# Kernel tuning notes

Hardware: AMD Instinct MI355X
Metric: run time of the kernel (lower is better)

The kernel has to match this reference:

```python
import jax, jax.numpy as jnp
from jax import lax
import numpy as np

B, S, D, P = 32, 1024, 512, 20  # batch, seq_len, feature_dim, positioning_embedding


def setup_inputs() -> dict:
    key = jax.random.key(0)
    ks = jax.random.split(key, 10)
    s = 0.1  # param scale
    return {
        "x": jax.random.normal(ks[0], (B, S, D), jnp.float32),
        "pad_lengths": jnp.full((B,), S, dtype=jnp.int32),
        # LSTM params (torch gate order i,f,g,o)
        "W_ih": jax.random.normal(ks[1], (4 * P, D), jnp.float32) * s,
        "W_hh": jax.random.normal(ks[2], (4 * P, P), jnp.float32) * s,
        "b_ih": jax.random.normal(ks[3], (4 * P,), jnp.float32) * s,
        "b_hh": jax.random.normal(ks[4], (4 * P,), jnp.float32) * s,
        # mu_generator: Linear(P, 3); sigma_generator: Linear(P, 1)
        "W_mu": jax.random.normal(ks[5], (3, P), jnp.float32) * s,
        "b_mu": jax.random.normal(ks[6], (3,), jnp.float32) * s,
        "W_sigma": jax.random.normal(ks[7], (1, P), jnp.float32) * s,
        "b_sigma": jax.random.normal(ks[8], (1,), jnp.float32) * s,
    }


def _lstm(x, W_ih, W_hh, b_ih, b_hh):
    # x: [B, S, D] -> hidden states [B, S, P] (torch nn.LSTM, batch_first)
    b, _, _ = x.shape
    h0 = jnp.zeros((b, P), x.dtype)
    c0 = jnp.zeros((b, P), x.dtype)

    def step(carry, xt):
        h, c = carry
        gates = xt @ W_ih.T + h @ W_hh.T + b_ih + b_hh  # [B, 4P]
        i, f, g, o = jnp.split(gates, 4, axis=-1)
        i = jax.nn.sigmoid(i)
        f = jax.nn.sigmoid(f)
        g = jnp.tanh(g)
        o = jax.nn.sigmoid(o)
        c = f * c + i * g
        h = o * jnp.tanh(c)
        return (h, c), h

    _, hs = lax.scan(step, (h0, c0), jnp.swapaxes(x, 0, 1))  # hs: [S, B, P]
    return jnp.swapaxes(hs, 0, 1)


def reference(x, pad_lengths, W_ih, W_hh, b_ih, b_hh, W_mu, b_mu, W_sigma, b_sigma):
    b, s, _ = x.shape
    invL = 1.0 / pad_lengths.astype(jnp.float32)  # [B]

    pw = _lstm(x, W_ih, W_hh, b_ih, b_hh)                    # [B, S, P]
    mu_w = jax.nn.relu(pw @ W_mu.T + b_mu)                    # [B, S, 3]
    sigma = jax.nn.sigmoid(pw @ W_sigma.T + b_sigma)[..., 0]  # [B, S]

    # Sequential mu recurrence: mu_j = max(mw0*prev_mu + mw1/L + mw2*(j+1)/L, j/L)
    js = jnp.arange(s, dtype=jnp.float32)

    def mu_step(prev_mu, inp):
        mw, j = inp  # mw: [B, 3]
        mu = mw[:, 0] * prev_mu + mw[:, 1] * invL + mw[:, 2] * (j + 1.0) * invL
        mu = jnp.maximum(mu, j * invL)
        return mu, mu

    _, mus = lax.scan(mu_step, jnp.zeros((b,), jnp.float32),
                      (jnp.swapaxes(mu_w, 0, 1), js))  # mus: [S, B]
    mus = mus.T  # [B, S]

    # Gaussian attention over positions k/L, causal mask k <= j, L1 normalize
    pos = js[None, :] * invL[:, None]                         # [B, S] = k/L
    d2 = (pos[:, None, :] - mus[:, :, None]) ** 2             # [B, S(j), S(k)]
    w = jnp.exp(-d2 / (2.0 * sigma[:, :, None] ** 2 + 0.001))
    causal = jnp.tril(jnp.ones((s, s), jnp.float32))          # k <= j
    w = w * causal[None]
    w = w / jnp.maximum(jnp.sum(jnp.abs(w), axis=-1, keepdims=True), 1e-12)
    context = jnp.einsum('bjk,bkd->bjd', w, x)                # [B, S, D]
    return context
```

## Files before the change

### kernel.cpp

```cpp
#include <hip/hip_runtime.h>
#include <hip/hip_bf16.h>

#define B_ 32
#define S_ 1024
#define D_ 512
#define P_ 20
#define G_ 80

typedef __attribute__((ext_vector_type(8))) short short8v;
typedef __attribute__((ext_vector_type(4))) float f32x4;

__device__ __forceinline__ float sigm_f(float x) { return 1.f / (1.f + __expf(-x)); }
__device__ __forceinline__ float tanh_f(float x) { return 1.f - 2.f / (__expf(2.f * x) + 1.f); }
__device__ __forceinline__ unsigned short f2bf(float f) {
    unsigned int u = __float_as_uint(f);
    u += 0x7FFF + ((u >> 16) & 1);
    return (unsigned short)(u >> 16);
}
__device__ __forceinline__ float bcast(float v, int lane) {
    return __uint_as_float(__builtin_amdgcn_readlane(__float_as_uint(v), lane));
}
__device__ __forceinline__ float swap32(float x, int l) {
    unsigned d = __float_as_uint(x);
    unsigned s = d;
    asm("v_permlane32_swap_b32 %0, %1" : "+v"(d), "+v"(s));
    return (l & 32) ? __uint_as_float(d) : __uint_as_float(s);
}
__device__ __forceinline__ short8v cvt8(float4 p, float4 q) {
    union { __hip_bfloat162 h2[4]; short8v s; } u;
    u.h2[0] = __float22bfloat162_rn(float2{p.x, p.y});
    u.h2[1] = __float22bfloat162_rn(float2{p.z, p.w});
    u.h2[2] = __float22bfloat162_rn(float2{q.x, q.y});
    u.h2[3] = __float22bfloat162_rn(float2{q.z, q.w});
    return u.s;
}

__global__ __launch_bounds__(256) void xw_kernel(const float* __restrict__ x,
                                                 const float* __restrict__ W_ih,
                                                 const float* __restrict__ b_ih,
                                                 const float* __restrict__ b_hh,
                                                 float* __restrict__ xw) {
    const int tid = threadIdx.x;
    const int w = tid >> 6, l = tid & 63;
    const int lo = l & 15, hi = l >> 4;
    const int m0 = blockIdx.x * 64 + w * 16;

    f32x4 acc[5];
#pragma unroll
    for (int n = 0; n < 5; ++n) acc[n] = (f32x4){0.f, 0.f, 0.f, 0.f};

    const float* xrow = x + (size_t)(m0 + lo) * D_ + hi * 8;
#pragma unroll 4
    for (int k0 = 0; k0 < D_; k0 += 32) {
        const float4 a0 = *(const float4*)(xrow + k0);
        const float4 a1 = *(const float4*)(xrow + k0 + 4);
        const short8v a = cvt8(a0, a1);
#pragma unroll
        for (int n = 0; n < 5; ++n) {
            const float* wr = W_ih + (size_t)(n * 16 + lo) * D_ + k0 + hi * 8;
            const float4 b0 = *(const float4*)(wr);
            const float4 b1 = *(const float4*)(wr + 4);
            const short8v bf = cvt8(b0, b1);
            acc[n] = __builtin_amdgcn_mfma_f32_16x16x32_bf16(a, bf, acc[n], 0, 0, 0);
        }
    }
#pragma unroll
    for (int n = 0; n < 5; ++n) {
        const int g = n * 16 + lo;
        const float bias = b_ih[g] + b_hh[g];
#pragma unroll
        for (int r = 0; r < 4; ++r) {
            const int m = m0 + hi * 4 + r;
            xw[(size_t)m * G_ + g] = acc[n][r] + bias;
        }
    }
}

__global__ __launch_bounds__(256) void conv_kernel(const float* __restrict__ x,
                                                   unsigned short* __restrict__ xT) {
    __shared__ unsigned short tile[64][80];
    const int b = blockIdx.z;
    const int s0 = blockIdx.x * 64;
    const int d0 = blockIdx.y * 64;
    const int t = threadIdx.x;
    const int r = t >> 2;
    const int c0 = (t & 3) * 16;

    const float4* src = (const float4*)(x + ((size_t)(b * S_ + s0 + r)) * D_ + d0 + c0);
    float4 v0 = src[0], v1 = src[1], v2 = src[2], v3 = src[3];
    float vv[16] = {v0.x, v0.y, v0.z, v0.w, v1.x, v1.y, v1.z, v1.w,
                    v2.x, v2.y, v2.z, v2.w, v3.x, v3.y, v3.z, v3.w};
#pragma unroll
    for (int e = 0; e < 16; ++e) tile[c0 + e][r] = f2bf(vv[e]);
    __syncthreads();

    const int dr = t >> 2;
    const int sc = (t & 3) * 16;
    const unsigned short* tr = &tile[dr][sc];
    uint4 w0 = *(const uint4*)(tr);
    uint4 w1 = *(const uint4*)(tr + 8);
    uint4* dst = (uint4*)(xT + ((size_t)(b * D_ + d0 + dr)) * S_ + s0 + sc);
    dst[0] = w0;
    dst[1] = w1;
}

__global__ __launch_bounds__(64) void lstm_kernel(const float* __restrict__ xw,
                                                  const float* __restrict__ W_hh,
                                                  const float* __restrict__ W_mu,
                                                  const float* __restrict__ b_mu,
                                                  const float* __restrict__ W_sig,
                                                  const float* __restrict__ b_sig,
                                                  const int* __restrict__ pad,
                                                  float* __restrict__ mus,
                                                  float* __restrict__ sigma) {
    const int b = blockIdx.x;
    const int l = threadIdx.x;
    __shared__ float mbuf[S_];
    __shared__ float sbuf[S_];

    float E[P_], F[P_];
#pragma unroll
    for (int q = 0; q < P_; ++q) { E[q] = 0.f; F[q] = 0.f; }
    if (l < P_) {
#pragma unroll
        for (int q = 0; q < P_; ++q) {
            E[q] = W_hh[(0 * P_ + l) * P_ + q];
            F[q] = W_hh[(1 * P_ + l) * P_ + q];
        }
    } else if (l < 23) {
#pragma unroll
        for (int q = 0; q < P_; ++q) E[q] = W_mu[(l - 20) * P_ + q];
    } else if (l == 23) {
#pragma unroll
        for (int q = 0; q < P_; ++q) E[q] = W_sig[q];
    } else if (l >= 32 && l < 32 + P_) {
        const int p = l - 32;
#pragma unroll
        for (int q = 0; q < P_; ++q) {
            E[q] = W_hh[(2 * P_ + p) * P_ + q];
            F[q] = W_hh[(3 * P_ + p) * P_ + q];
        }
    }

    const float invL = 1.f / (float)pad[b];
    const float hb = (l >= 20 && l < 23) ? b_mu[l - 20] : (l == 23 ? b_sig[0] : 0.f);
    const float ka = (l >= 32) ? 2.f : 1.f;
    const float Ka = (l >= 32) ? 2.f : 1.f;
    const float Kb = (l >= 32) ? -1.f : 0.f;
    const bool ld = (l < P_) || (l >= 32 && l < 32 + P_);
    const int o1 = (l < 32) ? l : (2 * P_ + (l - 32));
    const int o2 = (l < 32) ? (P_ + l) : (3 * P_ + (l - 32));

    float h = 0.f, c = 0.f, mu_prev = 0.f;
    const float* xwb = xw + (size_t)b * S_ * G_;

    float ri[8], rf[8];
#pragma unroll
    for (int u = 0; u < 8; ++u) {
        ri[u] = 0.f; rf[u] = 0.f;
        if (ld) {
            const float* r = xwb + (size_t)u * G_;
            ri[u] = r[o1]; rf[u] = r[o2];
        }
    }

    for (int T = 0; T < S_; T += 8) {
#pragma unroll
        for (int u = 0; u < 8; ++u) {
            const int t = T + u;
            float hq[P_];
#pragma unroll
            for (int q = 0; q < P_; ++q) hq[q] = bcast(h, q);

            float pa = 0.f, pb = 0.f, qa = 0.f, qb = 0.f;
#pragma unroll
            for (int q = 0; q < P_ / 2; ++q) {
                pa += E[q] * hq[q];            qa += F[q] * hq[q];
                pb += E[q + 10] * hq[q + 10];  qb += F[q + 10] * hq[q + 10];
            }
            const float arg1 = pa + pb + ri[u] + hb;
            const float arg2 = qa + qb + rf[u];

            const float s1 = sigm_f(ka * arg1);
            const float a1 = Ka * s1 + Kb;
            const float a2 = sigm_f(arg2);
            const float rv = fmaxf(arg1, 0.f);

            const float gx = swap32(a1, l);
            const float ox = swap32(a2, l);

            c = a2 * c + a1 * gx;
            h = ox * tanh_f(c);

            if (ld && t + 8 < S_) {
                const float* r = xwb + (size_t)(t + 8) * G_;
                ri[u] = r[o1]; rf[u] = r[o2];
            }
            if (t > 0) {
                const float s0v = bcast(rv, 20);
                const float s1v = bcast(rv, 21);
                const float s2v = bcast(rv, 22);
                const float j = (float)(t - 1);
                float m = s0v * mu_prev + (s1v + s2v * (j + 1.f)) * invL;
                m = fmaxf(m, j * invL);
                mu_prev = m;
                if (l == 0) mbuf[t - 1] = m;
                if (l == 23) sbuf[t - 1] = s1;
            }
        }
    }
    {
        float hq[P_];
#pragma unroll
        for (int q = 0; q < P_; ++q) hq[q] = bcast(h, q);
        float pa = 0.f, pb = 0.f;
#pragma unroll
        for (int q = 0; q < P_ / 2; ++q) {
            pa += E[q] * hq[q];
            pb += E[q + 10] * hq[q + 10];
        }
        const float arg1 = pa + pb + hb;
        if (l == 23) sbuf[S_ - 1] = sigm_f(arg1);
        const float rv = fmaxf(arg1, 0.f);
        const float s0v = bcast(rv, 20);
        const float s1v = bcast(rv, 21);
        const float s2v = bcast(rv, 22);
        const float j = (float)(S_ - 1);
        float m = s0v * mu_prev + (s1v + s2v * (j + 1.f)) * invL;
        m = fmaxf(m, j * invL);
        if (l == 0) mbuf[S_ - 1] = m;
    }
    __builtin_amdgcn_s_waitcnt(0);
#pragma unroll
    for (int i = 0; i < S_ / (64 * 4); ++i) {
        const int idx = (i * 64 + l) * 4;
        *(float4*)&mus[(size_t)b * S_ + idx] = *(const float4*)&mbuf[idx];
        *(float4*)&sigma[(size_t)b * S_ + idx] = *(const float4*)&sbuf[idx];
    }
}

__global__ __launch_bounds__(256, 2) void attn_kernel(const unsigned short* __restrict__ xT,
                                                      const float* __restrict__ mus,
                                                      const float* __restrict__ sigma,
                                                      const int* __restrict__ pad,
                                                      float* __restrict__ out) {
    __shared__ unsigned short xt[D_][40];
    __shared__ float rsm[4][16];

    const int jt = (gridDim.x - 1) - blockIdx.x;
    const int b = blockIdx.y;
    const int tid = threadIdx.x;
    const int w = tid >> 6;
    const int l = tid & 63;
    const int lo = l & 15, hi = l >> 4;
    const int jw0 = jt * 64 + w * 16;
    const float invL = 1.f / (float)pad[b];

    const int jA = jw0 + lo;
    const float mu = mus[(size_t)b * S_ + jA];
    const float sg = sigma[(size_t)b * S_ + jA];
    const float nis = -1.f / (2.f * sg * sg + 0.001f);

    f32x4 acc[32];
#pragma unroll
    for (int dt = 0; dt < 32; ++dt) acc[dt] = (f32x4){0.f, 0.f, 0.f, 0.f};

    const unsigned short* xTb = xT + (size_t)b * D_ * S_;
    float rs = 0.f;
    const int kend = (jt + 1) * 64;

    for (int k0 = 0; k0 < kend; k0 += 32) {
        uint4 v[2][4];
#pragma unroll
        for (int rr = 0; rr < 2; ++rr) {
            const int d = tid + rr * 256;
            const uint4* src = (const uint4*)(xTb + (size_t)d * S_ + k0);
#pragma unroll
            for (int i = 0; i < 4; ++i) v[rr][i] = src[i];
        }
        __syncthreads();
#pragma unroll
        for (int rr = 0; rr < 2; ++rr) {
            const int d = tid + rr * 256;
#pragma unroll
            for (int i = 0; i < 4; ++i) *(uint4*)&xt[d][i * 8] = v[rr][i];
        }
        __syncthreads();

        short8v a;
#pragma unroll
        for (int e = 0; e < 8; ++e) {
            const int k = k0 + hi * 8 + e;
            const float dd = (float)k * invL - mu;
            const float wv = (k <= jA) ? __expf(dd * dd * nis) : 0.f;
            rs += wv;
            a[e] = (short)f2bf(wv);
        }
#pragma unroll
        for (int dt = 0; dt < 32; ++dt) {
            const short8v bf = *(const short8v*)&xt[dt * 16 + lo][hi * 8];
            acc[dt] = __builtin_amdgcn_mfma_f32_16x16x32_bf16(a, bf, acc[dt], 0, 0, 0);
        }
    }

    rs += __shfl_xor(rs, 16);
    rs += __shfl_xor(rs, 32);
    if (l < 16) rsm[w][l] = rs;
    __syncthreads();

#pragma unroll
    for (int r = 0; r < 4; ++r) {
        const int j = jw0 + hi * 4 + r;
        const float rcp = 1.f / fmaxf(rsm[w][hi * 4 + r], 1e-12f);
        float* ob = out + ((size_t)b * S_ + j) * D_ + lo;
#pragma unroll
        for (int dt = 0; dt < 32; ++dt) {
            ob[dt * 16] = acc[dt][r] * rcp;
        }
    }
}

extern "C" void kernel_launch(void* const* d_in, const int* in_sizes, int n_in,
                              void* d_out, int out_size, void* d_ws, size_t ws_size,
                              hipStream_t stream) {
    const float* x     = (const float*)d_in[0];
    const int*   pad   = (const int*)d_in[1];
    const float* W_ih  = (const float*)d_in[2];
    const float* W_hh  = (const float*)d_in[3];
    const float* b_ih  = (const float*)d_in[4];
    const float* b_hh  = (const float*)d_in[5];
    const float* W_mu  = (const float*)d_in[6];
    const float* b_mu  = (const float*)d_in[7];
    const float* W_sig = (const float*)d_in[8];
    const float* b_sig = (const float*)d_in[9];
    float* out = (float*)d_out;

    float* xw    = (float*)d_ws;
    float* mus   = xw + (size_t)B_ * S_ * G_;
    float* sigma = mus + (size_t)B_ * S_;
    unsigned short* xT = (unsigned short*)(sigma + (size_t)B_ * S_);

    xw_kernel<<<(B_ * S_) / 64, 256, 0, stream>>>(x, W_ih, b_ih, b_hh, xw);
    conv_kernel<<<dim3(S_ / 64, D_ / 64, B_), 256, 0, stream>>>(x, xT);
    lstm_kernel<<<B_, 64, 0, stream>>>(xw, W_hh, W_mu, b_mu, W_sig, b_sig, pad, mus, sigma);
    attn_kernel<<<dim3(S_ / 64, B_), 256, 0, stream>>>(xT, mus, sigma, pad, out);
}
```

Measured before the change: 772.1 us.

## Stage LSTM input projections into LDS in 128-step chunks with vectorized loads

Instead of issuing per-step scalar global loads of the precomputed input gate projections, the LSTM recurrence kernel now bulk-loads 128 timesteps per chunk into shared memory with coalesced float4 loads, then reads each step's values from LDS. It also splits the hidden-state dot product into four partial accumulators to shorten the dependency chain. This aims to remove global-memory latency from the serial recurrence critical path, at the cost of a stall at each chunk boundary and 40KB of extra shared memory. The single-wavefront block relies on s_waitcnt rather than a barrier for visibility of the staged data.

```diff
diff --git a/kernel.cpp b/kernel.cpp
--- a/kernel.cpp
+++ b/kernel.cpp
@@ -117,6 +117,7 @@
     const int l = threadIdx.x;
     __shared__ float mbuf[S_];
     __shared__ float sbuf[S_];
+    __shared__ float stage[128 * G_];
 
     float E[P_], F[P_];
 #pragma unroll
@@ -152,63 +153,83 @@
     const int o2 = (l < 32) ? (P_ + l) : (3 * P_ + (l - 32));
 
     float h = 0.f, c = 0.f, mu_prev = 0.f;
-    const float* xwb = xw + (size_t)b * S_ * G_;
-
-    float ri[8], rf[8];
-#pragma unroll
-    for (int u = 0; u < 8; ++u) {
-        ri[u] = 0.f; rf[u] = 0.f;
-        if (ld) {
-            const float* r = xwb + (size_t)u * G_;
-            ri[u] = r[o1]; rf[u] = r[o2];
-        }
-    }
-
-    for (int T = 0; T < S_; T += 8) {
-#pragma unroll
-        for (int u = 0; u < 8; ++u) {
-            const int t = T + u;
-            float hq[P_];
-#pragma unroll
-            for (int q = 0; q < P_; ++q) hq[q] = bcast(h, q);
-
-            float pa = 0.f, pb = 0.f, qa = 0.f, qb = 0.f;
-#pragma unroll
-            for (int q = 0; q < P_ / 2; ++q) {
-                pa += E[q] * hq[q];            qa += F[q] * hq[q];
-                pb += E[q + 10] * hq[q + 10];  qb += F[q + 10] * hq[q + 10];
-            }
-            const float arg1 = pa + pb + ri[u] + hb;
-            const float arg2 = qa + qb + rf[u];
-
-            const float s1 = sigm_f(ka * arg1);
-            const float a1 = Ka * s1 + Kb;
-            const float a2 = sigm_f(arg2);
-            const float rv = fmaxf(arg1, 0.f);
-
-            const float gx = swap32(a1, l);
-            const float ox = swap32(a2, l);
-
-            c = a2 * c + a1 * gx;
-            h = ox * tanh_f(c);
-
-            if (ld && t + 8 < S_) {
-                const float* r = xwb + (size_t)(t + 8) * G_;
-                ri[u] = r[o1]; rf[u] = r[o2];
-            }
-            if (t > 0) {
-                const float s0v = bcast(rv, 20);
-                const float s1v = bcast(rv, 21);
-                const float s2v = bcast(rv, 22);
-                const float j = (float)(t - 1);
-                float m = s0v * mu_prev + (s1v + s2v * (j + 1.f)) * invL;
-                m = fmaxf(m, j * invL);
-                mu_prev = m;
-                if (l == 0) mbuf[t - 1] = m;
-                if (l == 23) sbuf[t - 1] = s1;
-            }
-        }
-    }
+    const float4* xwb4 = (const float4*)(xw + (size_t)b * S_ * G_);
+
+    float ri[4], rf[4];
+#pragma unroll
+    for (int u = 0; u < 4; ++u) { ri[u] = 0.f; rf[u] = 0.f; }
+
+    auto STEP = [&](int t, int u, int rrow) {
+        float hq[P_];
+#pragma unroll
+        for (int q = 0; q < P_; ++q) hq[q] = bcast(h, q);
+
+        float pa = 0.f, pb = 0.f, pc = 0.f, pd = 0.f;
+        float qa = 0.f, qb = 0.f, qc = 0.f, qd = 0.f;
+#pragma unroll
+        for (int q = 0; q < 5; ++q) {
+            pa += E[q]      * hq[q];       qa += F[q]      * hq[q];
+            pb += E[q + 5]  * hq[q + 5];   qb += F[q + 5]  * hq[q + 5];
+            pc += E[q + 10] * hq[q + 10];  qc += F[q + 10] * hq[q + 10];
+            pd += E[q + 15] * hq[q + 15];  qd += F[q + 15] * hq[q + 15];
+        }
+        const float arg1 = ((pa + pb) + (pc + pd)) + ri[u] + hb;
+        const float arg2 = ((qa + qb) + (qc + qd)) + rf[u];
+
+        const float s1 = sigm_f(ka * arg1);
+        const float a1 = Ka * s1 + Kb;
+        const float a2 = sigm_f(arg2);
+        const float rv = fmaxf(arg1, 0.f);
+
+        const float gx = swap32(a1, l);
+        const float ox = swap32(a2, l);
+
+        c = a2 * c + a1 * gx;
+        h = ox * tanh_f(c);
+
+        if (rrow >= 0 && ld) {
+            ri[u] = stage[rrow * G_ + o1];
+            rf[u] = stage[rrow * G_ + o2];
+        }
+        if (t > 0) {
+            const float s0v = bcast(rv, 20);
+            const float s1v = bcast(rv, 21);
+            const float s2v = bcast(rv, 22);
+            const float j = (float)(t - 1);
+            float m = s0v * mu_prev + (s1v + s2v * (j + 1.f)) * invL;
+            m = fmaxf(m, j * invL);
+            mu_prev = m;
+            if (l == 0) mbuf[t - 1] = m;
+            if (l == 23) sbuf[t - 1] = s1;
+        }
+    };
+
+    for (int ch = 0; ch < S_ / 128; ++ch) {
+        const int c0 = ch * 128;
+#pragma unroll
+        for (int g = 0; g < 2; ++g) {
+            float4 tmp[20];
+#pragma unroll
+            for (int k = 0; k < 20; ++k)
+                tmp[k] = xwb4[(size_t)c0 * (G_ / 4) + l + 64 * (g * 20 + k)];
+#pragma unroll
+            for (int k = 0; k < 20; ++k)
+                *(float4*)&stage[(l + 64 * (g * 20 + k)) * 4] = tmp[k];
+        }
+        __builtin_amdgcn_s_waitcnt(0);
+
+#pragma unroll
+        for (int u = 0; u < 4; ++u)
+            if (ld) { ri[u] = stage[u * G_ + o1]; rf[u] = stage[u * G_ + o2]; }
+
+        for (int T = 0; T < 124; T += 4) {
+#pragma unroll
+            for (int u = 0; u < 4; ++u) STEP(c0 + T + u, u, T + u + 4);
+        }
+#pragma unroll
+        for (int u = 0; u < 4; ++u) STEP(c0 + 124 + u, u, -1);
+    }
+
     {
         float hq[P_];
 #pragma unroll
```

New measurement: 849.2 us. +10.0%, slower.
